# Kernel tuning notes

Measured on AMD Instinct MI355X. Metric: run time of the kernel, lower is better.

## Reference

```python
import jax, jax.numpy as jnp
import numpy as np

# 47 skeleton edges (parent, child) from getSkeletalModelStructure()
EDGES = np.array([
    (0, 1), (1, 2), (2, 3), (3, 29), (1, 5), (5, 6), (6, 8), (8, 9), (8, 13),
    (8, 17), (8, 21), (8, 25), (9, 10), (10, 11), (11, 12), (13, 14), (14, 15),
    (15, 16), (17, 18), (18, 19), (19, 20), (21, 22), (22, 23), (23, 24),
    (25, 26), (26, 27), (27, 28), (29, 30), (29, 34), (29, 38), (29, 42),
    (29, 46), (30, 31), (31, 32), (32, 33), (34, 35), (35, 36), (36, 37),
    (38, 39), (39, 40), (40, 41), (42, 43), (43, 44), (44, 45), (46, 47),
    (47, 48), (48, 49)], dtype=np.int32)

N_JOINTS = 50
N_EDGES = 47


def _length_direct(pose):
    # pose: [B, T, 151]; drop counter channel, view as joints
    B, T = pose.shape[0], pose.shape[1]
    p = pose[..., :-1].reshape(B, T, N_JOINTS, 3)
    diff = p[:, :, EDGES[:, 0], :] - p[:, :, EDGES[:, 1], :]   # [B, T, 47, 3]
    length = jnp.linalg.norm(diff, axis=-1)                      # [B, T, 47]
    eps = jnp.finfo(pose.dtype).tiny
    direct = diff / (length + eps)[..., None]                    # [B, T, 47, 3]
    # torch stacks each [B,T,3] edge dir along dim=-1 -> [B,T,3,47], then reshapes
    directs = jnp.transpose(direct, (0, 1, 3, 2)).reshape(B, T, N_EDGES * 3)
    return length, directs


def setup_inputs() -> dict:
    key = jax.random.key(0)
    k1, k2 = jax.random.split(key)
    B, T, D = 128, 1024, 151
    preds = jax.random.normal(k1, (B, T, D), dtype=jnp.float32)
    targets = jax.random.normal(k2, (B, T, D), dtype=jnp.float32)
    return {"preds": preds, "targets": targets}


def reference(preds, targets):
    target_pad = 0.0
    mask = (targets != target_pad).astype(preds.dtype)           # [B, T, 151]
    preds_m = preds * mask
    targets_m = targets * mask
    _, preds_dir = _length_direct(preds_m)
    _, targets_dir = _length_direct(targets_m)
    preds_dir = preds_dir * mask[:, :, :N_EDGES * 3]
    targets_dir = targets_dir * mask[:, :, :N_EDGES * 3]
    # cfg: loss='l1' (mean abs), vel_loss='mse' (mean square), loss_scale=1.0
    l1 = jnp.mean(jnp.abs(preds_m - targets_m))
    vel_mse = jnp.mean(jnp.square(preds_dir - targets_dir))
    return l1 + 0.1 * vel_mse
```

## Files before the change

kernel.cpp:

```cpp
#include <hip/hip_runtime.h>


#define N_ROWS   (128 * 1024)
#define ROW      151
#define N_EDGES  47
#define GRID     2048
#define BLOCK    256
#define ROWS_PER_BLOCK 64
#define SUBS     4
#define SUB_ROWS 16
#define SUB_DW   (SUB_ROWS * ROW)
#define SUB_F4   (SUB_DW / 4)
#define SUB_TASKS (SUB_ROWS * N_EDGES)

#if __has_builtin(__builtin_amdgcn_rsqf)
__device__ __forceinline__ float fast_rsq(float x) { return __builtin_amdgcn_rsqf(x); }
#else
__device__ __forceinline__ float fast_rsq(float x) {
    float r; asm volatile("v_rsq_f32 %0, %1" : "=v"(r) : "v"(x)); return r;
}
#endif

struct f3 { float x, y, z; };
__device__ __forceinline__ f3 ldg3(const float* __restrict__ p) {
    return *reinterpret_cast<const f3*>(p);
}

#define E(p, c) ((unsigned)((p) * 3) | ((unsigned)((c) * 3) << 16))
__constant__ unsigned c_edge[N_EDGES] = {
    E(0,1),  E(1,2),  E(2,3),  E(3,29), E(1,5),  E(5,6),  E(6,8),  E(8,9),
    E(8,13), E(8,17), E(8,21), E(8,25), E(9,10), E(10,11),E(11,12),E(13,14),
    E(14,15),E(15,16),E(17,18),E(18,19),E(19,20),E(21,22),E(22,23),E(23,24),
    E(25,26),E(26,27),E(27,28),E(29,30),E(29,34),E(29,38),E(29,42),E(29,46),
    E(30,31),E(31,32),E(32,33),E(34,35),E(35,36),E(36,37),E(38,39),E(39,40),
    E(40,41),E(42,43),E(43,44),E(44,45),E(46,47),E(47,48),E(48,49)};

struct EdgeAddr { int aP[3], aC[3], aM[3]; };

__device__ __forceinline__ void acc_l1(float4 pv, float4 tv, float& l1) {
    float a0 = (tv.x != 0.f) ? pv.x : 0.f;
    float a1 = (tv.y != 0.f) ? pv.y : 0.f;
    float a2 = (tv.z != 0.f) ? pv.z : 0.f;
    float a3 = (tv.w != 0.f) ? pv.w : 0.f;
    l1 += fabsf(a0 - tv.x) + fabsf(a1 - tv.y)
        + fabsf(a2 - tv.z) + fabsf(a3 - tv.w);
}

__device__ __forceinline__ void edge_task(
        const float* __restrict__ bp, const float* __restrict__ bt,
        int aP, int aC, int aM, float& vel) {
    f3 tp = ldg3(bt + aP);
    f3 tc = ldg3(bt + aC);
    f3 pp = ldg3(bp + aP);
    f3 pc = ldg3(bp + aC);
    float mg0 = bt[aM], mg1 = bt[aM + 47], mg2 = bt[aM + 94];
    float apx = (tp.x != 0.f) ? pp.x : 0.f;
    float apy = (tp.y != 0.f) ? pp.y : 0.f;
    float apz = (tp.z != 0.f) ? pp.z : 0.f;
    float acx = (tc.x != 0.f) ? pc.x : 0.f;
    float acy = (tc.y != 0.f) ? pc.y : 0.f;
    float acz = (tc.z != 0.f) ? pc.z : 0.f;
    float pdx = apx - acx, pdy = apy - acy, pdz = apz - acz;
    float tdx = tp.x - tc.x, tdy = tp.y - tc.y, tdz = tp.z - tc.z;
    float pd2 = pdx * pdx + pdy * pdy + pdz * pdz;
    float td2 = tdx * tdx + tdy * tdy + tdz * tdz;
    float pinv = (pd2 > 0.f) ? fast_rsq(pd2) : 0.f;
    float tinv = (td2 > 0.f) ? fast_rsq(td2) : 0.f;
    float dx = pdx * pinv - tdx * tinv;
    float dy = pdy * pinv - tdy * tinv;
    float dz = pdz * pinv - tdz * tinv;
    float m0 = (mg0 != 0.f) ? 1.f : 0.f;
    float m1 = (mg1 != 0.f) ? 1.f : 0.f;
    float m2 = (mg2 != 0.f) ? 1.f : 0.f;
    vel += m0 * dx * dx + m1 * dy * dy + m2 * dz * dz;
}

__global__ __launch_bounds__(BLOCK, 4) void reg_loss_main(
        const float* __restrict__ preds, const float* __restrict__ targets,
        float* __restrict__ wsL, float* __restrict__ wsV) {
    __shared__ float redL[4], redV[4];

    const int t = threadIdx.x;
    const int lane = t & 63;
    const int wave = t >> 6;

    const long long slab = (long long)blockIdx.x * (ROWS_PER_BLOCK * ROW);
    const float* sp = preds + slab;
    const float* st = targets + slab;

    EdgeAddr ea;
#pragma unroll
    for (int k = 0; k < 3; ++k) {
        int task = t + k * 256;
        bool a = task < SUB_TASKS;
        int r = a ? task / N_EDGES : 0;
        int e = a ? task - r * N_EDGES : 0;
        int roff = r * ROW;
        unsigned pk = c_edge[e];
        ea.aP[k] = roff + (int)(pk & 0xffff);
        ea.aC[k] = roff + (int)(pk >> 16);
        ea.aM[k] = roff + e;
    }

    float l1 = 0.f, vel = 0.f;

#pragma unroll
    for (int sub = 0; sub < SUBS; ++sub) {
        const float* __restrict__ bp = sp + sub * SUB_DW;
        const float* __restrict__ bt = st + sub * SUB_DW;
        const float4* __restrict__ bp4 = reinterpret_cast<const float4*>(bp);
        const float4* __restrict__ bt4 = reinterpret_cast<const float4*>(bt);

#pragma unroll
        for (int k = 0; k < 3; ++k) {
            int i = t + k * 256;
            if (k < 2 || t < (SUB_F4 - 512)) {
                float4 pv = bp4[i];
                float4 tv = bt4[i];
                acc_l1(pv, tv, l1);
            }
        }

#pragma unroll
        for (int k = 0; k < 3; ++k) {
            if (k < 2 || t < (SUB_TASKS - 512)) {
                edge_task(bp, bt, ea.aP[k], ea.aC[k], ea.aM[k], vel);
            }
        }
    }

#pragma unroll
    for (int off = 32; off > 0; off >>= 1) {
        l1  += __shfl_down(l1, off);
        vel += __shfl_down(vel, off);
    }
    if (lane == 0) { redL[wave] = l1; redV[wave] = vel; }
    __syncthreads();
    if (t == 0) {
        wsL[blockIdx.x] = redL[0] + redL[1] + redL[2] + redL[3];
        wsV[blockIdx.x] = redV[0] + redV[1] + redV[2] + redV[3];
    }
}

__global__ __launch_bounds__(BLOCK) void reg_loss_finalize(
        const float* __restrict__ wsL, const float* __restrict__ wsV,
        float* __restrict__ out) {
    __shared__ double rl[4], rv[4];
    const int t = threadIdx.x;
    const int lane = t & 63;
    const int wave = t >> 6;
    double L = 0.0, V = 0.0;
    for (int k = t; k < GRID; k += BLOCK) { L += wsL[k]; V += wsV[k]; }
#pragma unroll
    for (int off = 32; off > 0; off >>= 1) {
        L += __shfl_down(L, off);
        V += __shfl_down(V, off);
    }
    if (lane == 0) { rl[wave] = L; rv[wave] = V; }
    __syncthreads();
    if (t == 0) {
        double Ls = rl[0] + rl[1] + rl[2] + rl[3];
        double Vs = rv[0] + rv[1] + rv[2] + rv[3];
        out[0] = (float)(Ls / ((double)N_ROWS * 151.0)
                       + 0.1 * (Vs / ((double)N_ROWS * 141.0)));
    }
}

extern "C" void kernel_launch(void* const* d_in, const int* in_sizes, int n_in,
                              void* d_out, int out_size, void* d_ws, size_t ws_size,
                              hipStream_t stream) {
    const float* preds   = (const float*)d_in[0];
    const float* targets = (const float*)d_in[1];
    float* wsL = (float*)d_ws;
    float* wsV = wsL + GRID;
    float* out = (float*)d_out;

    reg_loss_main<<<GRID, BLOCK, 0, stream>>>(preds, targets, wsL, wsV);
    reg_loss_finalize<<<1, BLOCK, 0, stream>>>(wsL, wsV, out);
}
```

Before: 183.6 us.

## Stage per-wave row chunks in LDS and gather edge joints from shared memory

Each wave now streams 8 rows at a time into its own shared-memory slice with coalesced float4 loads, accumulating L1 as it goes. The edge-direction gathers then read from LDS instead of issuing unaligned scattered global loads that re-fetch the same data. This removes the redundant global and cache gather traffic at the cost of about 38 KB of LDS per block, which may limit occupancy, and some bank conflicts on the strided joint reads. Work is reorganised per wave, with inactive edge slots masked by a multiplier.

```diff
diff --git a/kernel.cpp b/kernel.cpp
--- a/kernel.cpp
+++ b/kernel.cpp
@@ -6,12 +6,10 @@
 #define N_EDGES  47
 #define GRID     2048
 #define BLOCK    256
-#define ROWS_PER_BLOCK 64
-#define SUBS     4
-#define SUB_ROWS 16
-#define SUB_DW   (SUB_ROWS * ROW)
-#define SUB_F4   (SUB_DW / 4)
-#define SUB_TASKS (SUB_ROWS * N_EDGES)
+#define ROWS_PER_WAVE 8
+#define WAVE_DW  (ROWS_PER_WAVE * ROW)
+#define WAVE_F4  (WAVE_DW / 4)
+#define CHUNKS   2
 
 #if __has_builtin(__builtin_amdgcn_rsqf)
 __device__ __forceinline__ float fast_rsq(float x) { return __builtin_amdgcn_rsqf(x); }
@@ -20,11 +18,6 @@
     float r; asm volatile("v_rsq_f32 %0, %1" : "=v"(r) : "v"(x)); return r;
 }
 #endif
-
-struct f3 { float x, y, z; };
-__device__ __forceinline__ f3 ldg3(const float* __restrict__ p) {
-    return *reinterpret_cast<const f3*>(p);
-}
 
 #define E(p, c) ((unsigned)((p) * 3) | ((unsigned)((c) * 3) << 16))
 __constant__ unsigned c_edge[N_EDGES] = {
@@ -35,8 +28,6 @@
     E(30,31),E(31,32),E(32,33),E(34,35),E(35,36),E(36,37),E(38,39),E(39,40),
     E(40,41),E(42,43),E(43,44),E(44,45),E(46,47),E(47,48),E(48,49)};
 
-struct EdgeAddr { int aP[3], aC[3], aM[3]; };
-
 __device__ __forceinline__ void acc_l1(float4 pv, float4 tv, float& l1) {
     float a0 = (tv.x != 0.f) ? pv.x : 0.f;
     float a1 = (tv.y != 0.f) ? pv.y : 0.f;
@@ -46,86 +37,86 @@
         + fabsf(a2 - tv.z) + fabsf(a3 - tv.w);
 }
 
-__device__ __forceinline__ void edge_task(
-        const float* __restrict__ bp, const float* __restrict__ bt,
-        int aP, int aC, int aM, float& vel) {
-    f3 tp = ldg3(bt + aP);
-    f3 tc = ldg3(bt + aC);
-    f3 pp = ldg3(bp + aP);
-    f3 pc = ldg3(bp + aC);
-    float mg0 = bt[aM], mg1 = bt[aM + 47], mg2 = bt[aM + 94];
-    float apx = (tp.x != 0.f) ? pp.x : 0.f;
-    float apy = (tp.y != 0.f) ? pp.y : 0.f;
-    float apz = (tp.z != 0.f) ? pp.z : 0.f;
-    float acx = (tc.x != 0.f) ? pc.x : 0.f;
-    float acy = (tc.y != 0.f) ? pc.y : 0.f;
-    float acz = (tc.z != 0.f) ? pc.z : 0.f;
-    float pdx = apx - acx, pdy = apy - acy, pdz = apz - acz;
-    float tdx = tp.x - tc.x, tdy = tp.y - tc.y, tdz = tp.z - tc.z;
-    float pd2 = pdx * pdx + pdy * pdy + pdz * pdz;
-    float td2 = tdx * tdx + tdy * tdy + tdz * tdz;
-    float pinv = (pd2 > 0.f) ? fast_rsq(pd2) : 0.f;
-    float tinv = (td2 > 0.f) ? fast_rsq(td2) : 0.f;
-    float dx = pdx * pinv - tdx * tinv;
-    float dy = pdy * pinv - tdy * tinv;
-    float dz = pdz * pinv - tdz * tinv;
-    float m0 = (mg0 != 0.f) ? 1.f : 0.f;
-    float m1 = (mg1 != 0.f) ? 1.f : 0.f;
-    float m2 = (mg2 != 0.f) ? 1.f : 0.f;
-    vel += m0 * dx * dx + m1 * dy * dy + m2 * dz * dz;
-}
-
 __global__ __launch_bounds__(BLOCK, 4) void reg_loss_main(
         const float* __restrict__ preds, const float* __restrict__ targets,
         float* __restrict__ wsL, float* __restrict__ wsV) {
+    __shared__ float S[4][2 * WAVE_DW];
     __shared__ float redL[4], redV[4];
 
     const int t = threadIdx.x;
     const int lane = t & 63;
     const int wave = t >> 6;
+    float* __restrict__ P = &S[wave][0];
+    float* __restrict__ T = &S[wave][WAVE_DW];
 
-    const long long slab = (long long)blockIdx.x * (ROWS_PER_BLOCK * ROW);
-    const float* sp = preds + slab;
-    const float* st = targets + slab;
+    const int r = lane & 7;
+    const int g = lane >> 3;
 
-    EdgeAddr ea;
+    int aP[6], aC[6], aM[6];
+    float act[6];
 #pragma unroll
-    for (int k = 0; k < 3; ++k) {
-        int task = t + k * 256;
-        bool a = task < SUB_TASKS;
-        int r = a ? task / N_EDGES : 0;
-        int e = a ? task - r * N_EDGES : 0;
-        int roff = r * ROW;
-        unsigned pk = c_edge[e];
-        ea.aP[k] = roff + (int)(pk & 0xffff);
-        ea.aC[k] = roff + (int)(pk >> 16);
-        ea.aM[k] = roff + e;
+    for (int j = 0; j < 6; ++j) {
+        int e = g + 8 * j;
+        bool a = (e < N_EDGES);
+        int ec = a ? e : (N_EDGES - 1);
+        unsigned pk = c_edge[ec];
+        aP[j]  = r * ROW + (int)(pk & 0xffff);
+        aC[j]  = r * ROW + (int)(pk >> 16);
+        aM[j]  = r * ROW + ec;
+        act[j] = a ? 1.f : 0.f;
     }
 
+    const long long wid = (long long)blockIdx.x * 4 + wave;
     float l1 = 0.f, vel = 0.f;
 
 #pragma unroll
-    for (int sub = 0; sub < SUBS; ++sub) {
-        const float* __restrict__ bp = sp + sub * SUB_DW;
-        const float* __restrict__ bt = st + sub * SUB_DW;
-        const float4* __restrict__ bp4 = reinterpret_cast<const float4*>(bp);
-        const float4* __restrict__ bt4 = reinterpret_cast<const float4*>(bt);
+    for (int c = 0; c < CHUNKS; ++c) {
+        const float4* __restrict__ gp4 = reinterpret_cast<const float4*>(
+            preds + (wid * CHUNKS + c) * WAVE_DW);
+        const float4* __restrict__ gt4 = reinterpret_cast<const float4*>(
+            targets + (wid * CHUNKS + c) * WAVE_DW);
+        float4* __restrict__ P4 = reinterpret_cast<float4*>(P);
+        float4* __restrict__ T4 = reinterpret_cast<float4*>(T);
 
 #pragma unroll
-        for (int k = 0; k < 3; ++k) {
-            int i = t + k * 256;
-            if (k < 2 || t < (SUB_F4 - 512)) {
-                float4 pv = bp4[i];
-                float4 tv = bt4[i];
+        for (int k = 0; k < 5; ++k) {
+            int idx = lane + k * 64;
+            if (k < 4 || lane < (WAVE_F4 - 256)) {
+                float4 pv = gp4[idx];
+                float4 tv = gt4[idx];
+                P4[idx] = pv;
+                T4[idx] = tv;
                 acc_l1(pv, tv, l1);
             }
         }
 
 #pragma unroll
-        for (int k = 0; k < 3; ++k) {
-            if (k < 2 || t < (SUB_TASKS - 512)) {
-                edge_task(bp, bt, ea.aP[k], ea.aC[k], ea.aM[k], vel);
-            }
+        for (int j = 0; j < 6; ++j) {
+            int p = aP[j], q = aC[j], m = aM[j];
+            float tpx = T[p], tpy = T[p + 1], tpz = T[p + 2];
+            float tcx = T[q], tcy = T[q + 1], tcz = T[q + 2];
+            float ppx = P[p], ppy = P[p + 1], ppz = P[p + 2];
+            float pcx = P[q], pcy = P[q + 1], pcz = P[q + 2];
+            float mg0 = T[m], mg1 = T[m + 47], mg2 = T[m + 94];
+            float apx = (tpx != 0.f) ? ppx : 0.f;
+            float apy = (tpy != 0.f) ? ppy : 0.f;
+            float apz = (tpz != 0.f) ? ppz : 0.f;
+            float acx = (tcx != 0.f) ? pcx : 0.f;
+            float acy = (tcy != 0.f) ? pcy : 0.f;
+            float acz = (tcz != 0.f) ? pcz : 0.f;
+            float pdx = apx - acx, pdy = apy - acy, pdz = apz - acz;
+            float tdx = tpx - tcx, tdy = tpy - tcy, tdz = tpz - tcz;
+            float pd2 = pdx * pdx + pdy * pdy + pdz * pdz;
+            float td2 = tdx * tdx + tdy * tdy + tdz * tdz;
+            float pinv = (pd2 > 0.f) ? fast_rsq(pd2) : 0.f;
+            float tinv = (td2 > 0.f) ? fast_rsq(td2) : 0.f;
+            float dx = pdx * pinv - tdx * tinv;
+            float dy = pdy * pinv - tdy * tinv;
+            float dz = pdz * pinv - tdz * tinv;
+            float m0 = (mg0 != 0.f) ? act[j] : 0.f;
+            float m1 = (mg1 != 0.f) ? act[j] : 0.f;
+            float m2 = (mg2 != 0.f) ? act[j] : 0.f;
+            vel += m0 * dx * dx + m1 * dy * dy + m2 * dz * dz;
         }
     }
 
```

New measurement: 193.6 us. 1.05x slower.
